# Optimization experiments

Hardware: AMD Instinct MI355X
Metric: run time of the kernel (lower is better)

## Reference

```python
import jax, jax.numpy as jnp
import numpy as np

B = 131072      # batch
NC = 1000       # num_classes
A = 128         # action_dim
ELD = 128       # embedding_latent_dim
VQN = 512       # vq_num_embeddings
VQD = 64        # vq_embedding_dim
SQUISH = 1.0
CC = 0.25       # commitment cost

def _he(k, fi, fo):
    lim = float(np.sqrt(6.0 / fi))
    return jax.random.uniform(k, (fi, fo), jnp.float32, -lim, lim)

def setup_inputs() -> dict:
    key = jax.random.key(0)
    ks = jax.random.split(key, 16)
    cb_lim = float(np.sqrt(3.0 / VQD))  # variance_scaling fan_in uniform
    return {
        "obs": jax.random.randint(ks[0], (B,), 0, NC),
        "embed": jax.random.normal(ks[1], (NC, ELD), jnp.float32) * 0.02,
        "W1": _he(ks[2], ELD, 128), "b1": jnp.zeros((128,), jnp.float32),
        "W2": _he(ks[3], 128, 128), "b2": jnp.zeros((128,), jnp.float32),
        "W3": _he(ks[4], 128, 128), "b3": jnp.zeros((128,), jnp.float32),
        "Wp": _he(ks[5], 128, VQD), "bp": jnp.zeros((VQD,), jnp.float32),
        "codebook": jax.random.uniform(ks[6], (VQN, VQD), jnp.float32, -cb_lim, cb_lim),
        "Wa": jax.random.normal(ks[7], (VQD, A), jnp.float32) * 0.01, "ba": jnp.zeros((A,), jnp.float32),
        "Ws": jax.random.normal(ks[8], (VQD, A), jnp.float32) * 0.01, "bs": jnp.zeros((A,), jnp.float32),
        "Wc1": _he(ks[9], VQD, 128), "bc1": jnp.zeros((128,), jnp.float32),
        "Wc2": _he(ks[10], 128, 128), "bc2": jnp.zeros((128,), jnp.float32),
        "Wc3": _he(ks[11], 128, 32), "bc3": jnp.zeros((32,), jnp.float32),
        "Wc4": _he(ks[12], 32, 1), "bc4": jnp.zeros((1,), jnp.float32),
    }

def reference(obs, embed, W1, b1, W2, b2, W3, b3, Wp, bp, codebook,
              Wa, ba, Ws, bs, Wc1, bc1, Wc2, bc2, Wc3, bc3, Wc4, bc4):
    # embedding lookup + small dense stack
    y = jnp.take(embed, obs, axis=0)                 # [B, 128]
    z = jax.nn.relu(y @ W1 + b1)
    z = jax.nn.relu(z @ W2 + b2)
    z = jax.nn.relu(z @ W3 + b3)
    z = z @ Wp + bp                                  # [B, 64] project to vq dim
    # VQ: pairwise squared distances, argmin, gather (== one_hot @ codebook)
    d = (jnp.sum(z * z, axis=1, keepdims=True)
         - 2.0 * (z @ codebook.T)
         + jnp.sum(codebook * codebook, axis=1))     # [B, 512]
    idx = jnp.argmin(d, axis=1)                      # [B]
    quant = jnp.take(codebook, idx, axis=0)          # [B, 64]
    q = z + jax.lax.stop_gradient(quant - z)         # straight-through
    e_loss = jnp.mean((jax.lax.stop_gradient(q) - z) ** 2)
    q_loss = jnp.mean((q - jax.lax.stop_gradient(z)) ** 2)
    vq_loss = q_loss + CC * e_loss
    # actor heads (pi = MvNormalDiag(actor_mean, scale_diag); return params)
    actor_mean = jax.nn.sigmoid(q @ Wa + ba)
    scale_diag = jax.nn.sigmoid(q @ Ws + bs) * SQUISH + 1e-8
    # critic head
    c = jax.nn.sigmoid(q @ Wc1 + bc1)
    c = jax.nn.sigmoid(c @ Wc2 + bc2)
    c = jax.nn.sigmoid(c @ Wc3 + bc3)
    critic = jnp.squeeze(c @ Wc4 + bc4, axis=-1)     # [B]
    return actor_mean, scale_diag, critic, vq_loss, idx
```

## Files before the change

kernel.cpp:

```cpp
#include <hip/hip_runtime.h>
#include <math.h>


typedef float f4 __attribute__((ext_vector_type(4)));

__device__ __forceinline__ float sigmoidf_(float x){ return 1.0f/(1.0f + expf(-x)); }

__global__ __launch_bounds__(256) void transpose_cb_kernel(
    const float* __restrict__ cb, double* __restrict__ cbT, int VQN)
{
    int gid = blockIdx.x * 256 + threadIdx.x;
    int total = 64 * VQN;
    if (gid < total) {
        int j = gid / VQN;
        int k = gid - j * VQN;
        cbT[gid] = (double)cb[(size_t)k * 64 + j];
    }
}

__global__ __launch_bounds__(128) void per_class_kernel(
    const float* __restrict__ embed,
    const float* __restrict__ W1, const float* __restrict__ b1,
    const float* __restrict__ W2, const float* __restrict__ b2,
    const float* __restrict__ W3, const float* __restrict__ b3,
    const float* __restrict__ Wp, const float* __restrict__ bp,
    const float* __restrict__ cb, const double* __restrict__ cbT,
    const float* __restrict__ Wa, const float* __restrict__ ba,
    const float* __restrict__ Ws, const float* __restrict__ bs,
    const float* __restrict__ Wc1, const float* __restrict__ bc1,
    const float* __restrict__ Wc2, const float* __restrict__ bc2,
    const float* __restrict__ Wc3, const float* __restrict__ bc3,
    const float* __restrict__ Wc4, const float* __restrict__ bc4,
    float* __restrict__ am_t, float* __restrict__ sd_t,
    float* __restrict__ cr_t, int* __restrict__ idx_t, float* __restrict__ e_t,
    float* __restrict__ loss_slot, int VQN)
{
    const int c = blockIdx.x;
    const int t = threadIdx.x;
    if (c == 0 && t == 0) *loss_slot = 0.0f;

    __shared__ double Abuf[128];
    __shared__ double Bbuf[128];
    __shared__ double zp[64];
    __shared__ float  qv[64];
    __shared__ double rd[128];
    __shared__ int    ri[128];
    __shared__ float  h1[128], h2[128], h3[32];

    Abuf[t] = (double)embed[(size_t)c * 128 + t];
    __syncthreads();

    {
        double a0 = (double)b1[t], a1 = 0.0, a2 = 0.0, a3 = 0.0;
        for (int i = 0; i < 128; i += 4) {
            a0 = fma(Abuf[i+0], (double)W1[(i+0) * 128 + t], a0);
            a1 = fma(Abuf[i+1], (double)W1[(i+1) * 128 + t], a1);
            a2 = fma(Abuf[i+2], (double)W1[(i+2) * 128 + t], a2);
            a3 = fma(Abuf[i+3], (double)W1[(i+3) * 128 + t], a3);
        }
        double acc = (a0 + a1) + (a2 + a3);
        Bbuf[t] = acc > 0.0 ? acc : 0.0;
    }
    __syncthreads();

    {
        double a0 = (double)b2[t], a1 = 0.0, a2 = 0.0, a3 = 0.0;
        for (int i = 0; i < 128; i += 4) {
            a0 = fma(Bbuf[i+0], (double)W2[(i+0) * 128 + t], a0);
            a1 = fma(Bbuf[i+1], (double)W2[(i+1) * 128 + t], a1);
            a2 = fma(Bbuf[i+2], (double)W2[(i+2) * 128 + t], a2);
            a3 = fma(Bbuf[i+3], (double)W2[(i+3) * 128 + t], a3);
        }
        double acc = (a0 + a1) + (a2 + a3);
        Abuf[t] = acc > 0.0 ? acc : 0.0;
    }
    __syncthreads();

    {
        double a0 = (double)b3[t], a1 = 0.0, a2 = 0.0, a3 = 0.0;
        for (int i = 0; i < 128; i += 4) {
            a0 = fma(Abuf[i+0], (double)W3[(i+0) * 128 + t], a0);
            a1 = fma(Abuf[i+1], (double)W3[(i+1) * 128 + t], a1);
            a2 = fma(Abuf[i+2], (double)W3[(i+2) * 128 + t], a2);
            a3 = fma(Abuf[i+3], (double)W3[(i+3) * 128 + t], a3);
        }
        double acc = (a0 + a1) + (a2 + a3);
        Bbuf[t] = acc > 0.0 ? acc : 0.0;
    }
    __syncthreads();

    if (t < 64) {
        double a0 = (double)bp[t], a1 = 0.0, a2 = 0.0, a3 = 0.0;
        for (int i = 0; i < 128; i += 4) {
            a0 = fma(Bbuf[i+0], (double)Wp[(i+0) * 64 + t], a0);
            a1 = fma(Bbuf[i+1], (double)Wp[(i+1) * 64 + t], a1);
            a2 = fma(Bbuf[i+2], (double)Wp[(i+2) * 64 + t], a2);
            a3 = fma(Bbuf[i+3], (double)Wp[(i+3) * 64 + t], a3);
        }
        zp[t] = (a0 + a1) + (a2 + a3);
    }
    __syncthreads();

    double best = 1e300; int bidx = 0;
    if (VQN == 512) {
        const double* base = cbT + t;
        double a0e = 0.0, a0o = 0.0, a1e = 0.0, a1o = 0.0;
        double a2e = 0.0, a2o = 0.0, a3e = 0.0, a3o = 0.0;
        for (int j = 0; j < 64; j += 2) {
            const double* r0 = base + (size_t)j * 512;
            const double* r1 = r0 + 512;
            double z0 = zp[j], z1 = zp[j+1];
            double d;
            d = z0 - r0[0];    a0e = fma(d, d, a0e);
            d = z1 - r1[0];    a0o = fma(d, d, a0o);
            d = z0 - r0[128];  a1e = fma(d, d, a1e);
            d = z1 - r1[128];  a1o = fma(d, d, a1o);
            d = z0 - r0[256];  a2e = fma(d, d, a2e);
            d = z1 - r1[256];  a2o = fma(d, d, a2o);
            d = z0 - r0[384];  a3e = fma(d, d, a3e);
            d = z1 - r1[384];  a3o = fma(d, d, a3o);
        }
        double s0 = a0e + a0o, s1 = a1e + a1o, s2 = a2e + a2o, s3 = a3e + a3o;
        best = s0; bidx = t;
        if (s1 < best) { best = s1; bidx = t + 128; }
        if (s2 < best) { best = s2; bidx = t + 256; }
        if (s3 < best) { best = s3; bidx = t + 384; }
    } else {
        for (int k = t; k < VQN; k += 128) {
            const float* crow = cb + (size_t)k * 64;
            double s0 = 0.0, s1 = 0.0;
            for (int j = 0; j < 64; j += 2) {
                double d0 = zp[j+0] - (double)crow[j+0];
                double d1 = zp[j+1] - (double)crow[j+1];
                s0 = fma(d0, d0, s0);
                s1 = fma(d1, d1, s1);
            }
            double s = s0 + s1;
            if (s < best) { best = s; bidx = k; }
        }
    }
    rd[t] = best; ri[t] = bidx;
    __syncthreads();
    for (int sft = 64; sft > 0; sft >>= 1) {
        if (t < sft) {
            if (rd[t + sft] < rd[t] || (rd[t + sft] == rd[t] && ri[t + sft] < ri[t])) {
                rd[t] = rd[t + sft]; ri[t] = ri[t + sft];
            }
        }
        __syncthreads();
    }
    const int widx = ri[0];
    if (t < 64) qv[t] = cb[(size_t)widx * 64 + t];
    __syncthreads();

    {
        float la0 = ba[t],  la1 = 0.0f;
        float ls0 = bs[t],  ls1 = 0.0f;
        float l10 = bc1[t], l11 = 0.0f;
        for (int j = 0; j < 64; j += 2) {
            float q0 = qv[j], q1 = qv[j+1];
            la0 = fmaf(q0, Wa[j * 128 + t], la0);
            la1 = fmaf(q1, Wa[(j+1) * 128 + t], la1);
            ls0 = fmaf(q0, Ws[j * 128 + t], ls0);
            ls1 = fmaf(q1, Ws[(j+1) * 128 + t], ls1);
            l10 = fmaf(q0, Wc1[j * 128 + t], l10);
            l11 = fmaf(q1, Wc1[(j+1) * 128 + t], l11);
        }
        am_t[(size_t)c * 128 + t] = sigmoidf_(la0 + la1);
        sd_t[(size_t)c * 128 + t] = sigmoidf_(ls0 + ls1) * 1.0f + 1e-8f;
        h1[t] = sigmoidf_(l10 + l11);
    }
    __syncthreads();

    {
        float l20 = bc2[t], l21 = 0.0f;
        for (int i = 0; i < 128; i += 2) {
            l20 = fmaf(h1[i],   Wc2[i * 128 + t],     l20);
            l21 = fmaf(h1[i+1], Wc2[(i+1) * 128 + t], l21);
        }
        h2[t] = sigmoidf_(l20 + l21);
    }
    __syncthreads();

    if (t < 32) {
        float l30 = bc3[t], l31 = 0.0f;
        for (int i = 0; i < 128; i += 2) {
            l30 = fmaf(h2[i],   Wc3[i * 32 + t],     l30);
            l31 = fmaf(h2[i+1], Wc3[(i+1) * 32 + t], l31);
        }
        h3[t] = sigmoidf_(l30 + l31);
    }
    __syncthreads();

    if (t == 0) {
        float l4 = bc4[0];
        for (int i = 0; i < 32; ++i) l4 = fmaf(h3[i], Wc4[i], l4);
        cr_t[c] = l4;
        idx_t[c] = widx;
        double e0 = 0.0, e1 = 0.0;
        for (int j = 0; j < 64; j += 2) {
            double d0 = (double)qv[j]   - zp[j];
            double d1 = (double)qv[j+1] - zp[j+1];
            e0 = fma(d0, d0, e0); e1 = fma(d1, d1, e1);
        }
        e_t[c] = (float)(e0 + e1);
    }
}

__global__ __launch_bounds__(256) void scatter_kernel(
    const int* __restrict__ obs,
    const f4* __restrict__ am_t, const f4* __restrict__ sd_t,
    const float* __restrict__ cr_t, const int* __restrict__ idx_t,
    const float* __restrict__ e_t,
    f4* __restrict__ out_vec, float* __restrict__ out_critic,
    float* __restrict__ out_idx, float* __restrict__ out_loss,
    int B, float scale)
{
    __shared__ float red[256];
    const int vecBlocks = (2 * B * 32) / 256;
    if ((int)blockIdx.x < vecBlocks) {
        int gid = blockIdx.x * 256 + threadIdx.x;
        int half = B * 32;
        if (gid < half) {
            int b = gid >> 5;
            int j = gid & 31;
            __builtin_nontemporal_store(am_t[(size_t)obs[b] * 32 + j], &out_vec[gid]);
        } else {
            int g = gid - half;
            int b = g >> 5;
            int j = g & 31;
            __builtin_nontemporal_store(sd_t[(size_t)obs[b] * 32 + j], &out_vec[gid]);
        }
        return;
    }
    int b = (blockIdx.x - vecBlocks) * 256 + threadIdx.x;
    float e = 0.0f;
    if (b < B) {
        int o = obs[b];
        __builtin_nontemporal_store(cr_t[o], &out_critic[b]);
        __builtin_nontemporal_store((float)idx_t[o], &out_idx[b]);
        e = e_t[o];
    }
    red[threadIdx.x] = e;
    __syncthreads();
    for (int s = 128; s > 0; s >>= 1) {
        if (threadIdx.x < s) red[threadIdx.x] += red[threadIdx.x + s];
        __syncthreads();
    }
    if (threadIdx.x == 0) atomicAdd(out_loss, red[0] * scale);
}

extern "C" void kernel_launch(void* const* d_in, const int* in_sizes, int n_in,
                              void* d_out, int out_size, void* d_ws, size_t ws_size,
                              hipStream_t stream)
{
    const int*   obs   = (const int*)  d_in[0];
    const float* embed = (const float*)d_in[1];
    const float* W1    = (const float*)d_in[2];
    const float* b1    = (const float*)d_in[3];
    const float* W2    = (const float*)d_in[4];
    const float* b2    = (const float*)d_in[5];
    const float* W3    = (const float*)d_in[6];
    const float* b3    = (const float*)d_in[7];
    const float* Wp    = (const float*)d_in[8];
    const float* bp    = (const float*)d_in[9];
    const float* cb    = (const float*)d_in[10];
    const float* Wa    = (const float*)d_in[11];
    const float* ba    = (const float*)d_in[12];
    const float* Ws    = (const float*)d_in[13];
    const float* bs    = (const float*)d_in[14];
    const float* Wc1   = (const float*)d_in[15];
    const float* bc1   = (const float*)d_in[16];
    const float* Wc2   = (const float*)d_in[17];
    const float* bc2   = (const float*)d_in[18];
    const float* Wc3   = (const float*)d_in[19];
    const float* bc3   = (const float*)d_in[20];
    const float* Wc4   = (const float*)d_in[21];
    const float* bc4   = (const float*)d_in[22];

    const int B   = in_sizes[0];
    const int NC  = in_sizes[1] / 128;
    const int VQN = in_sizes[10] / 64;

    double* cbT  = (double*)d_ws;
    float*  am_t = (float*)(cbT + (size_t)64 * VQN);
    float*  sd_t = am_t + (size_t)NC * 128;
    float*  cr_t = sd_t + (size_t)NC * 128;
    float*  e_t  = cr_t + NC;
    int*    idx_t = (int*)(e_t + NC);

    float* out = (float*)d_out;
    const size_t cr_off   = (size_t)B * 256;
    const size_t loss_off = cr_off + (size_t)B;
    const size_t idx_off  = loss_off + 1;

    transpose_cb_kernel<<<(64 * VQN + 255) / 256, 256, 0, stream>>>(cb, cbT, VQN);

    per_class_kernel<<<NC, 128, 0, stream>>>(
        embed, W1, b1, W2, b2, W3, b3, Wp, bp, cb, cbT,
        Wa, ba, Ws, bs, Wc1, bc1, Wc2, bc2, Wc3, bc3, Wc4, bc4,
        am_t, sd_t, cr_t, idx_t, e_t, out + loss_off, VQN);

    const int vecBlocks    = (2 * B * 32) / 256;
    const int scalarBlocks = (B + 255) / 256;
    scatter_kernel<<<vecBlocks + scalarBlocks, 256, 0, stream>>>(
        obs, (const f4*)am_t, (const f4*)sd_t, cr_t, idx_t, e_t,
        (f4*)out, out + cr_off, out + idx_off, out + loss_off,
        B, 1.25f / ((float)B * 64.0f));
}
```

Baseline: 257.1 us.

## Split per-class MLP reductions across 256 threads and merge actor scatter stores

The per-class kernel now runs 256 threads per block. Each half computes a partial dot product over half of the input dimension, and the halves are combined through shared memory, which adds extra barriers. The VQ distance search is spread across 256 threads with two codes each. Separately, the scatter kernel now has each thread read the obs index once and write both the actor_mean and scale_diag vectors, which halves the vector blocks and the redundant obs reads.

```diff
diff --git a/kernel.cpp b/kernel.cpp
--- a/kernel.cpp
+++ b/kernel.cpp
@@ -18,7 +18,7 @@
     }
 }
 
-__global__ __launch_bounds__(128) void per_class_kernel(
+__global__ __launch_bounds__(256) void per_class_kernel(
     const float* __restrict__ embed,
     const float* __restrict__ W1, const float* __restrict__ b1,
     const float* __restrict__ W2, const float* __restrict__ b2,
@@ -35,77 +35,88 @@
     float* __restrict__ cr_t, int* __restrict__ idx_t, float* __restrict__ e_t,
     float* __restrict__ loss_slot, int VQN)
 {
-    const int c = blockIdx.x;
-    const int t = threadIdx.x;
-    if (c == 0 && t == 0) *loss_slot = 0.0f;
+    const int c   = blockIdx.x;
+    const int tid = threadIdx.x;
+    const int t   = tid & 127;
+    const int h   = tid >> 7;
+    const int i0  = h * 64;
+    if (c == 0 && tid == 0) *loss_slot = 0.0f;
 
     __shared__ double Abuf[128];
     __shared__ double Bbuf[128];
+    __shared__ double part[2][128];
     __shared__ double zp[64];
     __shared__ float  qv[64];
-    __shared__ double rd[128];
-    __shared__ int    ri[128];
+    __shared__ double rd[256];
+    __shared__ int    ri[256];
+    __shared__ float  fpart[2][128];
+    __shared__ float  gpart[2][128];
+    __shared__ float  hpart[2][128];
     __shared__ float  h1[128], h2[128], h3[32];
 
-    Abuf[t] = (double)embed[(size_t)c * 128 + t];
-    __syncthreads();
-
-    {
-        double a0 = (double)b1[t], a1 = 0.0, a2 = 0.0, a3 = 0.0;
-        for (int i = 0; i < 128; i += 4) {
+    if (h == 0) Abuf[t] = (double)embed[(size_t)c * 128 + t];
+    __syncthreads();
+
+    {
+        double a0 = (h == 0) ? (double)b1[t] : 0.0, a1 = 0.0, a2 = 0.0, a3 = 0.0;
+        for (int i = i0; i < i0 + 64; i += 4) {
             a0 = fma(Abuf[i+0], (double)W1[(i+0) * 128 + t], a0);
             a1 = fma(Abuf[i+1], (double)W1[(i+1) * 128 + t], a1);
             a2 = fma(Abuf[i+2], (double)W1[(i+2) * 128 + t], a2);
             a3 = fma(Abuf[i+3], (double)W1[(i+3) * 128 + t], a3);
         }
-        double acc = (a0 + a1) + (a2 + a3);
-        Bbuf[t] = acc > 0.0 ? acc : 0.0;
-    }
-    __syncthreads();
-
-    {
-        double a0 = (double)b2[t], a1 = 0.0, a2 = 0.0, a3 = 0.0;
-        for (int i = 0; i < 128; i += 4) {
+        part[h][t] = (a0 + a1) + (a2 + a3);
+    }
+    __syncthreads();
+    if (h == 0) { double acc = part[0][t] + part[1][t]; Bbuf[t] = acc > 0.0 ? acc : 0.0; }
+    __syncthreads();
+
+    {
+        double a0 = (h == 0) ? (double)b2[t] : 0.0, a1 = 0.0, a2 = 0.0, a3 = 0.0;
+        for (int i = i0; i < i0 + 64; i += 4) {
             a0 = fma(Bbuf[i+0], (double)W2[(i+0) * 128 + t], a0);
             a1 = fma(Bbuf[i+1], (double)W2[(i+1) * 128 + t], a1);
             a2 = fma(Bbuf[i+2], (double)W2[(i+2) * 128 + t], a2);
             a3 = fma(Bbuf[i+3], (double)W2[(i+3) * 128 + t], a3);
         }
-        double acc = (a0 + a1) + (a2 + a3);
-        Abuf[t] = acc > 0.0 ? acc : 0.0;
-    }
-    __syncthreads();
-
-    {
-        double a0 = (double)b3[t], a1 = 0.0, a2 = 0.0, a3 = 0.0;
-        for (int i = 0; i < 128; i += 4) {
+        part[h][t] = (a0 + a1) + (a2 + a3);
+    }
+    __syncthreads();
+    if (h == 0) { double acc = part[0][t] + part[1][t]; Abuf[t] = acc > 0.0 ? acc : 0.0; }
+    __syncthreads();
+
+    {
+        double a0 = (h == 0) ? (double)b3[t] : 0.0, a1 = 0.0, a2 = 0.0, a3 = 0.0;
+        for (int i = i0; i < i0 + 64; i += 4) {
             a0 = fma(Abuf[i+0], (double)W3[(i+0) * 128 + t], a0);
             a1 = fma(Abuf[i+1], (double)W3[(i+1) * 128 + t], a1);
             a2 = fma(Abuf[i+2], (double)W3[(i+2) * 128 + t], a2);
             a3 = fma(Abuf[i+3], (double)W3[(i+3) * 128 + t], a3);
         }
-        double acc = (a0 + a1) + (a2 + a3);
-        Bbuf[t] = acc > 0.0 ? acc : 0.0;
-    }
+        part[h][t] = (a0 + a1) + (a2 + a3);
+    }
+    __syncthreads();
+    if (h == 0) { double acc = part[0][t] + part[1][t]; Bbuf[t] = acc > 0.0 ? acc : 0.0; }
     __syncthreads();
 
     if (t < 64) {
-        double a0 = (double)bp[t], a1 = 0.0, a2 = 0.0, a3 = 0.0;
-        for (int i = 0; i < 128; i += 4) {
+        double a0 = (h == 0) ? (double)bp[t] : 0.0, a1 = 0.0, a2 = 0.0, a3 = 0.0;
+        for (int i = i0; i < i0 + 64; i += 4) {
             a0 = fma(Bbuf[i+0], (double)Wp[(i+0) * 64 + t], a0);
             a1 = fma(Bbuf[i+1], (double)Wp[(i+1) * 64 + t], a1);
             a2 = fma(Bbuf[i+2], (double)Wp[(i+2) * 64 + t], a2);
             a3 = fma(Bbuf[i+3], (double)Wp[(i+3) * 64 + t], a3);
         }
-        zp[t] = (a0 + a1) + (a2 + a3);
-    }
+        part[h][t] = (a0 + a1) + (a2 + a3);
+    }
+    __syncthreads();
+    if (h == 0 && t < 64) zp[t] = part[0][t] + part[1][t];
     __syncthreads();
 
     double best = 1e300; int bidx = 0;
     if (VQN == 512) {
-        const double* base = cbT + t;
+        const double* base = cbT + tid;
         double a0e = 0.0, a0o = 0.0, a1e = 0.0, a1o = 0.0;
-        double a2e = 0.0, a2o = 0.0, a3e = 0.0, a3o = 0.0;
         for (int j = 0; j < 64; j += 2) {
             const double* r0 = base + (size_t)j * 512;
             const double* r1 = r0 + 512;
@@ -113,20 +124,14 @@
             double d;
             d = z0 - r0[0];    a0e = fma(d, d, a0e);
             d = z1 - r1[0];    a0o = fma(d, d, a0o);
-            d = z0 - r0[128];  a1e = fma(d, d, a1e);
-            d = z1 - r1[128];  a1o = fma(d, d, a1o);
-            d = z0 - r0[256];  a2e = fma(d, d, a2e);
-            d = z1 - r1[256];  a2o = fma(d, d, a2o);
-            d = z0 - r0[384];  a3e = fma(d, d, a3e);
-            d = z1 - r1[384];  a3o = fma(d, d, a3o);
-        }
-        double s0 = a0e + a0o, s1 = a1e + a1o, s2 = a2e + a2o, s3 = a3e + a3o;
-        best = s0; bidx = t;
-        if (s1 < best) { best = s1; bidx = t + 128; }
-        if (s2 < best) { best = s2; bidx = t + 256; }
-        if (s3 < best) { best = s3; bidx = t + 384; }
+            d = z0 - r0[256];  a1e = fma(d, d, a1e);
+            d = z1 - r1[256];  a1o = fma(d, d, a1o);
+        }
+        double s0 = a0e + a0o, s1 = a1e + a1o;
+        best = s0; bidx = tid;
+        if (s1 < best) { best = s1; bidx = tid + 256; }
     } else {
-        for (int k = t; k < VQN; k += 128) {
+        for (int k = tid; k < VQN; k += 256) {
             const float* crow = cb + (size_t)k * 64;
             double s0 = 0.0, s1 = 0.0;
             for (int j = 0; j < 64; j += 2) {
@@ -139,25 +144,26 @@
             if (s < best) { best = s; bidx = k; }
         }
     }
-    rd[t] = best; ri[t] = bidx;
-    __syncthreads();
-    for (int sft = 64; sft > 0; sft >>= 1) {
-        if (t < sft) {
-            if (rd[t + sft] < rd[t] || (rd[t + sft] == rd[t] && ri[t + sft] < ri[t])) {
-                rd[t] = rd[t + sft]; ri[t] = ri[t + sft];
+    rd[tid] = best; ri[tid] = bidx;
+    __syncthreads();
+    for (int sft = 128; sft > 0; sft >>= 1) {
+        if (tid < sft) {
+            if (rd[tid + sft] < rd[tid] || (rd[tid + sft] == rd[tid] && ri[tid + sft] < ri[tid])) {
+                rd[tid] = rd[tid + sft]; ri[tid] = ri[tid + sft];
             }
         }
         __syncthreads();
     }
     const int widx = ri[0];
-    if (t < 64) qv[t] = cb[(size_t)widx * 64 + t];
-    __syncthreads();
-
-    {
-        float la0 = ba[t],  la1 = 0.0f;
-        float ls0 = bs[t],  ls1 = 0.0f;
-        float l10 = bc1[t], l11 = 0.0f;
-        for (int j = 0; j < 64; j += 2) {
+    if (tid < 64) qv[tid] = cb[(size_t)widx * 64 + tid];
+    __syncthreads();
+
+    {
+        const int j0 = h * 32;
+        float la0 = (h == 0) ? ba[t]  : 0.0f, la1 = 0.0f;
+        float ls0 = (h == 0) ? bs[t]  : 0.0f, ls1 = 0.0f;
+        float l10 = (h == 0) ? bc1[t] : 0.0f, l11 = 0.0f;
+        for (int j = j0; j < j0 + 32; j += 2) {
             float q0 = qv[j], q1 = qv[j+1];
             la0 = fmaf(q0, Wa[j * 128 + t], la0);
             la1 = fmaf(q1, Wa[(j+1) * 128 + t], la1);
@@ -166,33 +172,43 @@
             l10 = fmaf(q0, Wc1[j * 128 + t], l10);
             l11 = fmaf(q1, Wc1[(j+1) * 128 + t], l11);
         }
-        am_t[(size_t)c * 128 + t] = sigmoidf_(la0 + la1);
-        sd_t[(size_t)c * 128 + t] = sigmoidf_(ls0 + ls1) * 1.0f + 1e-8f;
-        h1[t] = sigmoidf_(l10 + l11);
-    }
-    __syncthreads();
-
-    {
-        float l20 = bc2[t], l21 = 0.0f;
-        for (int i = 0; i < 128; i += 2) {
-            l20 = fmaf(h1[i],   Wc2[i * 128 + t],     l20);
-            l21 = fmaf(h1[i+1], Wc2[(i+1) * 128 + t], l21);
-        }
-        h2[t] = sigmoidf_(l20 + l21);
-    }
+        fpart[h][t] = la0 + la1;
+        gpart[h][t] = ls0 + ls1;
+        hpart[h][t] = l10 + l11;
+    }
+    __syncthreads();
+    if (h == 0) {
+        am_t[(size_t)c * 128 + t] = sigmoidf_(fpart[0][t] + fpart[1][t]);
+        sd_t[(size_t)c * 128 + t] = sigmoidf_(gpart[0][t] + gpart[1][t]) * 1.0f + 1e-8f;
+        h1[t] = sigmoidf_(hpart[0][t] + hpart[1][t]);
+    }
+    __syncthreads();
+
+    {
+        float l0 = (h == 0) ? bc2[t] : 0.0f, l1 = 0.0f;
+        for (int i = i0; i < i0 + 64; i += 2) {
+            l0 = fmaf(h1[i],   Wc2[i * 128 + t],     l0);
+            l1 = fmaf(h1[i+1], Wc2[(i+1) * 128 + t], l1);
+        }
+        fpart[h][t] = l0 + l1;
+    }
+    __syncthreads();
+    if (h == 0) h2[t] = sigmoidf_(fpart[0][t] + fpart[1][t]);
     __syncthreads();
 
     if (t < 32) {
-        float l30 = bc3[t], l31 = 0.0f;
-        for (int i = 0; i < 128; i += 2) {
-            l30 = fmaf(h2[i],   Wc3[i * 32 + t],     l30);
-            l31 = fmaf(h2[i+1], Wc3[(i+1) * 32 + t], l31);
-        }
-        h3[t] = sigmoidf_(l30 + l31);
-    }
-    __syncthreads();
-
-    if (t == 0) {
+        float l0 = (h == 0) ? bc3[t] : 0.0f, l1 = 0.0f;
+        for (int i = i0; i < i0 + 64; i += 2) {
+            l0 = fmaf(h2[i],   Wc3[i * 32 + t],     l0);
+            l1 = fmaf(h2[i+1], Wc3[(i+1) * 32 + t], l1);
+        }
+        fpart[h][t] = l0 + l1;
+    }
+    __syncthreads();
+    if (h == 0 && t < 32) h3[t] = sigmoidf_(fpart[0][t] + fpart[1][t]);
+    __syncthreads();
+
+    if (tid == 0) {
         float l4 = bc4[0];
         for (int i = 0; i < 32; ++i) l4 = fmaf(h3[i], Wc4[i], l4);
         cr_t[c] = l4;
@@ -217,20 +233,14 @@
     int B, float scale)
 {
     __shared__ float red[256];
-    const int vecBlocks = (2 * B * 32) / 256;
+    const int vecBlocks = (B * 32) / 256;
     if ((int)blockIdx.x < vecBlocks) {
         int gid = blockIdx.x * 256 + threadIdx.x;
-        int half = B * 32;
-        if (gid < half) {
-            int b = gid >> 5;
-            int j = gid & 31;
-            __builtin_nontemporal_store(am_t[(size_t)obs[b] * 32 + j], &out_vec[gid]);
-        } else {
-            int g = gid - half;
-            int b = g >> 5;
-            int j = g & 31;
-            __builtin_nontemporal_store(sd_t[(size_t)obs[b] * 32 + j], &out_vec[gid]);
-        }
+        int b = gid >> 5;
+        int j = gid & 31;
+        size_t row = (size_t)obs[b] * 32 + j;
+        __builtin_nontemporal_store(am_t[row], &out_vec[gid]);
+        __builtin_nontemporal_store(sd_t[row], &out_vec[(size_t)B * 32 + gid]);
         return;
     }
     int b = (blockIdx.x - vecBlocks) * 256 + threadIdx.x;
@@ -296,12 +306,12 @@
 
     transpose_cb_kernel<<<(64 * VQN + 255) / 256, 256, 0, stream>>>(cb, cbT, VQN);
 
-    per_class_kernel<<<NC, 128, 0, stream>>>(
+    per_class_kernel<<<NC, 256, 0, stream>>>(
         embed, W1, b1, W2, b2, W3, b3, Wp, bp, cb, cbT,
         Wa, ba, Ws, bs, Wc1, bc1, Wc2, bc2, Wc3, bc3, Wc4, bc4,
         am_t, sd_t, cr_t, idx_t, e_t, out + loss_off, VQN);
 
-    const int vecBlocks    = (2 * B * 32) / 256;
+    const int vecBlocks    = (B * 32) / 256;
     const int scalarBlocks = (B + 255) / 256;
     scatter_kernel<<<vecBlocks + scalarBlocks, 256, 0, stream>>>(
         obs, (const f4*)am_t, (const f4*)sd_t, cr_t, idx_t, e_t,
```

After: 378.3 us. +47.2%, slower.
